# Performance work log

Hardware: AMD Instinct MI355X
Metric: run time of the kernel (lower is better)

The kernel has to match this reference:

```python
import jax, jax.numpy as jnp
import numpy as np

KSIZE, H, W = 11, 256, 256
IN_C, OUT_C, B = 3, 64, 4


def _foveated_coords(height, width, k):
    """Integer foveated sampling coords [H, W, k, k] for y and x.

    Ring scale per kernel tap: Chebyshev dist from center -> 1/3/5/7.
    Matches FoveatedSamplingConv2d._create_all_foveated_kernels, where
    coords are exact integers, so bilinear grid_sample == integer gather.
    """
    c = k // 2
    ki = np.arange(k)
    dist = np.maximum(np.abs(ki[:, None] - c), np.abs(ki[None, :] - c))  # [k,k]
    scale = np.where(dist <= 1, 1, np.where(dist == 2, 3, np.where(dist == 3, 5, 7)))
    off_y = (ki[:, None] - c) * scale  # [k,k]
    off_x = (ki[None, :] - c) * scale  # [k,k]
    yy = np.arange(height)[:, None, None, None]
    xx = np.arange(width)[None, :, None, None]
    sy = np.clip(yy + off_y[None, None], 0, height - 1)  # [H,W,k,k]
    sx = np.clip(xx + off_x[None, None], 0, width - 1)   # [H,W,k,k]
    return jnp.asarray(sy, jnp.int32), jnp.asarray(sx, jnp.int32)


def setup_inputs() -> dict:
    key = jax.random.key(0)
    k1, k2, k3 = jax.random.split(key, 3)
    x = jax.random.normal(k1, (B, IN_C, H, W), dtype=jnp.float32)
    # Kaiming-uniform-ish init scale (exact distribution irrelevant for correctness)
    fan_in = IN_C * KSIZE * KSIZE
    bound = 1.0 / np.sqrt(fan_in)
    weight = jax.random.uniform(k2, (OUT_C, IN_C, KSIZE, KSIZE), dtype=jnp.float32,
                                minval=-bound, maxval=bound)
    bias = jax.random.uniform(k3, (OUT_C,), dtype=jnp.float32, minval=-bound, maxval=bound)
    sy, sx = _foveated_coords(H, W, KSIZE)
    return {"x": x, "weight": weight, "bias": bias, "sy": sy, "sx": sx}


def reference(x, weight, bias, sy, sx):
    # Irregular gather: sampled[b,c,h,w,ki,kj] = x[b,c, sy[h,w,ki,kj], sx[h,w,ki,kj]]
    sampled = x[:, :, sy, sx]  # [B, C, H, W, k, k]
    out = jnp.einsum('bchwkl,ockl->bohw', sampled, weight)
    return out + bias[None, :, None, None]
```

## Files before the change

kernel.cpp:

```cpp
#include <hip/hip_runtime.h>


#define HH 256
#define WW 256
#define INC 3
#define OC 64
#define KS 11
#define BB 4
#define NKC 12
#define PH 326
#define PW 512
#define PAD 35
#define NDY 23
#define NROW 69
#define ROWB 672
#define ROWU16 336

typedef __attribute__((ext_vector_type(4))) float f32x4;
typedef __attribute__((ext_vector_type(8))) short s16x8;
typedef unsigned int u32;
typedef unsigned short u16;

static __device__ const int dyv[NDY] = {
    -35, -28, -21, -15, -14, -10, -7, -6, -5, -3, -1,
      0,   1,   3,   5,   6,   7, 10, 14, 15, 21, 28, 35};

static __device__ __forceinline__ u16 f2bf(float f) {
    u32 u = __builtin_bit_cast(u32, f);
    u32 r = (u + 0x7FFFu + ((u >> 16) & 1u)) >> 16;
    return (u16)r;
}

__global__ void __launch_bounds__(256)
prep_fused(const float* __restrict__ x, const float* __restrict__ w,
           u16* __restrict__ xs, u16* __restrict__ wf) {
    const int tid = threadIdx.x;
    if (blockIdx.x < 96) {
        int i = blockIdx.x * 256 + tid;
        int j    = i & 7;
        int lane = (i >> 3) & 63;
        int ot   = (i >> 9) & 3;
        int kc   = i >> 11;
        int o  = ot * 16 + (lane & 15);
        int k  = kc * 32 + ((lane >> 4) << 3) + j;
        int c  = k >> 7;
        int tt = k & 127;
        float val = 0.f;
        if (tt < 121) {
            int ky = tt / 11, kx = tt % 11;
            val = w[((o * INC + c) * KS + ky) * KS + kx];
        }
        wf[i] = f2bf(val);
    } else {
        const int pb = blockIdx.x - 96;
        const int k  = pb & 7;
        const int i  = pb >> 3;
        const int r  = i * 2 + (tid >> 7);
        if (r < 3 * 163) {
            const int c   = r / 163;
            const int pz  = r - c * 163;
            const int py  = (k & 1) * 163 + pz;
            const int b   = k >> 1;
            const int px0 = (tid & 127) * 4;
            const int sy  = min(max(py - PAD, 0), HH - 1);
            const float* src = x + (((size_t)b * INC + c) * HH + sy) * WW;
            ushort4 o4;
            int s0 = min(max(px0 + 0 - PAD, 0), WW - 1);
            int s1 = min(max(px0 + 1 - PAD, 0), WW - 1);
            int s2 = min(max(px0 + 2 - PAD, 0), WW - 1);
            int s3 = min(max(px0 + 3 - PAD, 0), WW - 1);
            o4.x = f2bf(src[s0]); o4.y = f2bf(src[s1]);
            o4.z = f2bf(src[s2]); o4.w = f2bf(src[s3]);
            *(ushort4*)&xs[(((size_t)b * INC + c) * PH + py) * PW + px0] = o4;
        }
    }
}

__global__ void __launch_bounds__(256, 3)
fov_lds(const u16* __restrict__ xs, const u16* __restrict__ wf,
        const float* __restrict__ bias, float* __restrict__ out) {
    __shared__ __align__(16) u16 sdata[NROW * ROWU16];
    __shared__ u32 offL[NKC * 32];

    const int tid  = threadIdx.x;
    const int lane = tid & 63;
    const int wv   = tid >> 6;
    const int obid = (blockIdx.x & 7) * 128 + (blockIdx.x >> 3);
    const int b = obid >> 8;
    const int h = obid & 255;

    for (int t = tid; t < NKC * 32; t += 256) {
        int c = t >> 7, tt = t & 127;
        u32 v = 0;
        if (tt < 121) {
            int ky = tt / 11, kx = tt - (tt / 11) * 11;
            int ay = ky - 5, ax = kx - 5;
            int d = max(abs(ay), abs(ax));
            int sc = (d <= 1) ? 1 : (d == 2 ? 3 : (d == 3 ? 5 : 7));
            int dy = ay * sc, dx = ax * sc;
            int di = 0;
#pragma unroll
            for (int s = 0; s < NDY; ++s) if (dyv[s] == dy) di = s;
            v = (u32)((c * NDY + di) * ROWB + (PAD + dx) * 2);
        }
        offL[t] = v;
    }

    for (int ri = wv; ri < NROW; ri += 4) {
        int c  = (ri >= 2 * NDY) ? 2 : (ri >= NDY ? 1 : 0);
        int di = ri - c * NDY;
        int py = h + PAD + dyv[di];
        const char* src = (const char*)(xs + (((size_t)b * INC + c) * PH + py) * PW);
        if (lane < ROWB / 16) {
            __builtin_amdgcn_global_load_lds(
                (const __attribute__((address_space(1))) void*)(src + lane * 16),
                (__attribute__((address_space(3))) void*)&sdata[ri * ROWU16],
                16, 0, 0);
        }
    }
    __syncthreads();

    const int g16 = lane & 15;
    const int kg  = lane >> 4;
    const u32 lane_base = (u32)((wv * 64 + 4 * g16) * 2);
    const u32* s32 = (const u32*)sdata;
    const s16x8* wbase = (const s16x8*)wf;

    f32x4 acc[4][4];
#pragma unroll
    for (int T = 0; T < 4; ++T)
#pragma unroll
        for (int ob = 0; ob < 4; ++ob) acc[T][ob] = (f32x4){0, 0, 0, 0};

    s16x8 A[2][4];
    {
        const s16x8* wp = wbase + lane;
        A[0][0] = wp[0]; A[0][1] = wp[64]; A[0][2] = wp[128]; A[0][3] = wp[192];
    }

#pragma unroll
    for (int kc = 0; kc < NKC; ++kc) {
        const int cur = kc & 1;
        const int nxt = cur ^ 1;
        if (kc + 1 < NKC) {
            const s16x8* wp = wbase + (((kc + 1) << 8) + lane);
            A[nxt][0] = wp[0];   A[nxt][1] = wp[64];
            A[nxt][2] = wp[128]; A[nxt][3] = wp[192];
        }
        const uint4* lp = (const uint4*)&offL[kc * 32 + kg * 8];
        const uint4 oA = lp[0], oB = lp[1];
        const u32 offs[8] = {oA.x, oA.y, oA.z, oA.w, oB.x, oB.y, oB.z, oB.w};
        u32 lo[8], hi[8];
#pragma unroll
        for (int j = 0; j < 8; ++j) {
            u32 addr = lane_base + offs[j];
            u32 i0 = addr >> 2;
            u32 sh = (addr & 2) << 3;
            u32 w0 = s32[i0], w1 = s32[i0 + 1], w2 = s32[i0 + 2];
            lo[j] = __builtin_amdgcn_alignbit(w1, w0, sh);
            hi[j] = __builtin_amdgcn_alignbit(w2, w1, sh);
        }
        __builtin_amdgcn_s_setprio(1);
#pragma unroll
        for (int T = 0; T < 4; ++T) {
            const u32 sel = (T & 1) ? 0x07060302u : 0x05040100u;
            const bool up = (T >> 1) != 0;
            union { u32 u[4]; s16x8 v; } bu;
            bu.u[0] = __builtin_amdgcn_perm(up ? hi[1] : lo[1], up ? hi[0] : lo[0], sel);
            bu.u[1] = __builtin_amdgcn_perm(up ? hi[3] : lo[3], up ? hi[2] : lo[2], sel);
            bu.u[2] = __builtin_amdgcn_perm(up ? hi[5] : lo[5], up ? hi[4] : lo[4], sel);
            bu.u[3] = __builtin_amdgcn_perm(up ? hi[7] : lo[7], up ? hi[6] : lo[6], sel);

            acc[T][0] = __builtin_amdgcn_mfma_f32_16x16x32_bf16(A[cur][0], bu.v, acc[T][0], 0, 0, 0);
            acc[T][1] = __builtin_amdgcn_mfma_f32_16x16x32_bf16(A[cur][1], bu.v, acc[T][1], 0, 0, 0);
            acc[T][2] = __builtin_amdgcn_mfma_f32_16x16x32_bf16(A[cur][2], bu.v, acc[T][2], 0, 0, 0);
            acc[T][3] = __builtin_amdgcn_mfma_f32_16x16x32_bf16(A[cur][3], bu.v, acc[T][3], 0, 0, 0);
        }
        __builtin_amdgcn_s_setprio(0);
    }

    const int orow = kg << 2;
    const float4* bp = (const float4*)bias;
#pragma unroll
    for (int ob = 0; ob < 4; ++ob) {
        const float4 bb = bp[ob * 4 + kg];
        const float bv[4] = {bb.x, bb.y, bb.z, bb.w};
#pragma unroll
        for (int r = 0; r < 4; ++r) {
            const int o = ob * 16 + orow + r;
            f32x4 st;
            st[0] = acc[0][ob][r] + bv[r];
            st[1] = acc[1][ob][r] + bv[r];
            st[2] = acc[2][ob][r] + bv[r];
            st[3] = acc[3][ob][r] + bv[r];
            float* op = out + (((size_t)b * OC + o) * HH + h) * WW + wv * 64 + 4 * g16;
            __builtin_nontemporal_store(st, (f32x4*)op);
        }
    }
}

__global__ void fovconv_transpose_w(const float* __restrict__ w,
                                    float* __restrict__ wT) {
    int i = blockIdx.x * 256 + threadIdx.x;
    const int N = OC * INC * KS * KS;
    if (i < N) {
        int o  = i / (INC * KS * KS);
        int ct = i % (INC * KS * KS);
        wT[ct * OC + o] = w[i];
    }
}

__global__ void __launch_bounds__(256)
fovconv_main(const float* __restrict__ x, const float* __restrict__ wT,
             const float* __restrict__ bias, float* __restrict__ out) {
    const int wpix = threadIdx.x;
    const int h    = blockIdx.x & (HH - 1);
    const int b    = blockIdx.x >> 8;
    float acc[OC];
#pragma unroll
    for (int o = 0; o < OC; ++o) acc[o] = 0.f;
    const float* xbp = x + (size_t)b * INC * HH * WW;
    for (int k = 0; k < KS; ++k) {
        const int dy = k - 5;
        for (int l = 0; l < KS; ++l) {
            const int dx = l - 5;
            const int d  = max(abs(dy), abs(dx));
            const int scale = (d <= 1) ? 1 : (d == 2 ? 3 : (d == 3 ? 5 : 7));
            const int sy = min(max(h + dy * scale, 0), HH - 1);
            const int sx = min(max(wpix + dx * scale, 0), WW - 1);
            const int base = sy * WW + sx;
            const int t = k * KS + l;
#pragma unroll
            for (int c = 0; c < INC; ++c) {
                const float xv = xbp[c * (HH * WW) + base];
                const float* wp = wT + (c * (KS * KS) + t) * OC;
#pragma unroll
                for (int o = 0; o < OC; ++o)
                    acc[o] = fmaf(xv, wp[o], acc[o]);
            }
        }
    }
    float* op = out + (((size_t)b * OC) * HH + h) * WW + wpix;
#pragma unroll
    for (int o = 0; o < OC; ++o)
        op[(size_t)o * HH * WW] = acc[o] + bias[o];
}

extern "C" void kernel_launch(void* const* d_in, const int* in_sizes, int n_in,
                              void* d_out, int out_size, void* d_ws, size_t ws_size,
                              hipStream_t stream) {
    const float* x    = (const float*)d_in[0];
    const float* wgt  = (const float*)d_in[1];
    const float* bias = (const float*)d_in[2];
    float* out = (float*)d_out;

    const size_t xs_bytes = (size_t)BB * INC * PH * PW * 2;
    const size_t wf_bytes = (size_t)NKC * 4 * 64 * 8 * 2;

    if (ws_size >= xs_bytes + wf_bytes) {
        u16* xsb = (u16*)d_ws;
        u16* wf  = (u16*)((char*)d_ws + xs_bytes);
        prep_fused<<<96 + 245 * 8, 256, 0, stream>>>(x, wgt, xsb, wf);
        fov_lds<<<BB * HH, 256, 0, stream>>>(xsb, wf, bias, out);
    } else {
        float* wT = (float*)d_ws;
        const int NW = OC * INC * KS * KS;
        fovconv_transpose_w<<<(NW + 255) / 256, 256, 0, stream>>>(wgt, wT);
        fovconv_main<<<BB * HH, 256, 0, stream>>>(x, wT, bias, out);
    }
}
```

Measured before the change: 38.24 us.

## Fuse input padding and bf16 conversion into the main conv kernel's LDS staging

Removes the separate pass that wrote a padded bf16 copy of the input to global memory. Each block now reads fp32 rows straight from x, clamps the coordinates, converts pairs to bf16 and stores them into LDS, with the row stride widened to 684 bytes. This drops one kernel's global write and read traffic. In exchange, staging uses per-thread scalar gathers with integer division instead of async 16-byte global-to-LDS copies, and each input row is reread by many blocks.

```diff
diff --git a/kernel.cpp b/kernel.cpp
--- a/kernel.cpp
+++ b/kernel.cpp
@@ -8,13 +8,11 @@
 #define KS 11
 #define BB 4
 #define NKC 12
-#define PH 326
-#define PW 512
 #define PAD 35
 #define NDY 23
 #define NROW 69
-#define ROWB 672
-#define ROWU16 336
+#define ROWB 684
+#define ROWPAIRS 171
 
 typedef __attribute__((ext_vector_type(4))) float f32x4;
 typedef __attribute__((ext_vector_type(8))) short s16x8;
@@ -32,54 +30,28 @@
 }
 
 __global__ void __launch_bounds__(256)
-prep_fused(const float* __restrict__ x, const float* __restrict__ w,
-           u16* __restrict__ xs, u16* __restrict__ wf) {
-    const int tid = threadIdx.x;
-    if (blockIdx.x < 96) {
-        int i = blockIdx.x * 256 + tid;
-        int j    = i & 7;
-        int lane = (i >> 3) & 63;
-        int ot   = (i >> 9) & 3;
-        int kc   = i >> 11;
-        int o  = ot * 16 + (lane & 15);
-        int k  = kc * 32 + ((lane >> 4) << 3) + j;
-        int c  = k >> 7;
-        int tt = k & 127;
-        float val = 0.f;
-        if (tt < 121) {
-            int ky = tt / 11, kx = tt % 11;
-            val = w[((o * INC + c) * KS + ky) * KS + kx];
-        }
-        wf[i] = f2bf(val);
-    } else {
-        const int pb = blockIdx.x - 96;
-        const int k  = pb & 7;
-        const int i  = pb >> 3;
-        const int r  = i * 2 + (tid >> 7);
-        if (r < 3 * 163) {
-            const int c   = r / 163;
-            const int pz  = r - c * 163;
-            const int py  = (k & 1) * 163 + pz;
-            const int b   = k >> 1;
-            const int px0 = (tid & 127) * 4;
-            const int sy  = min(max(py - PAD, 0), HH - 1);
-            const float* src = x + (((size_t)b * INC + c) * HH + sy) * WW;
-            ushort4 o4;
-            int s0 = min(max(px0 + 0 - PAD, 0), WW - 1);
-            int s1 = min(max(px0 + 1 - PAD, 0), WW - 1);
-            int s2 = min(max(px0 + 2 - PAD, 0), WW - 1);
-            int s3 = min(max(px0 + 3 - PAD, 0), WW - 1);
-            o4.x = f2bf(src[s0]); o4.y = f2bf(src[s1]);
-            o4.z = f2bf(src[s2]); o4.w = f2bf(src[s3]);
-            *(ushort4*)&xs[(((size_t)b * INC + c) * PH + py) * PW + px0] = o4;
-        }
-    }
+prep_wfrag(const float* __restrict__ w, u16* __restrict__ wf) {
+    int i = blockIdx.x * 256 + threadIdx.x;
+    int j    = i & 7;
+    int lane = (i >> 3) & 63;
+    int ot   = (i >> 9) & 3;
+    int kc   = i >> 11;
+    int o  = ot * 16 + (lane & 15);
+    int k  = kc * 32 + ((lane >> 4) << 3) + j;
+    int c  = k >> 7;
+    int tt = k & 127;
+    float val = 0.f;
+    if (tt < 121) {
+        int ky = tt / 11, kx = tt % 11;
+        val = w[((o * INC + c) * KS + ky) * KS + kx];
+    }
+    wf[i] = f2bf(val);
 }
 
 __global__ void __launch_bounds__(256, 3)
-fov_lds(const u16* __restrict__ xs, const u16* __restrict__ wf,
-        const float* __restrict__ bias, float* __restrict__ out) {
-    __shared__ __align__(16) u16 sdata[NROW * ROWU16];
+fov_fused(const float* __restrict__ x, const u16* __restrict__ wf,
+          const float* __restrict__ bias, float* __restrict__ out) {
+    __shared__ u32 sbuf[NROW * ROWPAIRS];
     __shared__ u32 offL[NKC * 32];
 
     const int tid  = threadIdx.x;
@@ -106,16 +78,20 @@
         offL[t] = v;
     }
 
-    for (int ri = wv; ri < NROW; ri += 4) {
-        int c  = (ri >= 2 * NDY) ? 2 : (ri >= NDY ? 1 : 0);
-        int di = ri - c * NDY;
-        int py = h + PAD + dyv[di];
-        const char* src = (const char*)(xs + (((size_t)b * INC + c) * PH + py) * PW);
-        if (lane < ROWB / 16) {
-            __builtin_amdgcn_global_load_lds(
-                (const __attribute__((address_space(1))) void*)(src + lane * 16),
-                (__attribute__((address_space(3))) void*)&sdata[ri * ROWU16],
-                16, 0, 0);
+    {
+        const float* xb = x + (size_t)b * (INC * HH * WW);
+        for (int i = tid; i < NROW * ROWPAIRS; i += 256) {
+            int row = i / ROWPAIRS;
+            int pr  = i - row * ROWPAIRS;
+            int c   = row / NDY;
+            int di  = row - c * NDY;
+            int sy  = min(max(h + dyv[di], 0), HH - 1);
+            int px0 = pr * 2;
+            int s0  = min(max(px0 - PAD, 0), WW - 1);
+            int s1  = min(max(px0 + 1 - PAD, 0), WW - 1);
+            const float* src = xb + ((size_t)c * HH + sy) * WW;
+            u32 pk = (u32)f2bf(src[s0]) | ((u32)f2bf(src[s1]) << 16);
+            sbuf[row * ROWPAIRS + pr] = pk;
         }
     }
     __syncthreads();
@@ -123,7 +99,7 @@
     const int g16 = lane & 15;
     const int kg  = lane >> 4;
     const u32 lane_base = (u32)((wv * 64 + 4 * g16) * 2);
-    const u32* s32 = (const u32*)sdata;
+    const u32* s32 = sbuf;
     const s16x8* wbase = (const s16x8*)wf;
 
     f32x4 acc[4][4];
@@ -254,14 +230,12 @@
     const float* bias = (const float*)d_in[2];
     float* out = (float*)d_out;
 
-    const size_t xs_bytes = (size_t)BB * INC * PH * PW * 2;
     const size_t wf_bytes = (size_t)NKC * 4 * 64 * 8 * 2;
 
-    if (ws_size >= xs_bytes + wf_bytes) {
-        u16* xsb = (u16*)d_ws;
-        u16* wf  = (u16*)((char*)d_ws + xs_bytes);
-        prep_fused<<<96 + 245 * 8, 256, 0, stream>>>(x, wgt, xsb, wf);
-        fov_lds<<<BB * HH, 256, 0, stream>>>(xsb, wf, bias, out);
+    if (ws_size >= wf_bytes) {
+        u16* wf = (u16*)d_ws;
+        prep_wfrag<<<96, 256, 0, stream>>>(wgt, wf);
+        fov_fused<<<BB * HH, 256, 0, stream>>>(x, wf, bias, out);
     } else {
         float* wT = (float*)d_ws;
         const int NW = OC * INC * KS * KS;
```

Measured after the change: 53.84 us. 40.8% more time.
